# Kernel tuning notes

Hardware: AMD Instinct MI355X
Metric: run time of the kernel (lower is better)

## Reference

```python
import jax, jax.numpy as jnp
import numpy as np
import math

B, S, D = 2, 2048, 2048
H, KVH, HD = 16, 8, 128  # n_heads, n_kv_heads, head_dim
N_REP = H // KVH
ROPE_THETA = 500000.0
NEG_INF = -1e9


def _rope(t, f):
    # t: (B,S,nh,HD) viewed as pairs; f: (S,HD//2,2) = (cos,sin)
    tp = t.reshape(*t.shape[:-1], HD // 2, 2)          # (B,S,nh,HD//2,2)
    fb = f[:, None]                                     # (S,1,HD//2,2)
    row1 = (tp * fb).sum(-1)                            # x0*c + x1*s
    f_rot = jnp.stack([fb[..., 1], -fb[..., 0]], axis=-1)  # (s, -c)
    row0 = (tp * f_rot).sum(-1)                         # x0*s - x1*c
    return jnp.stack([row0, row1], axis=-1).reshape(t.shape)


def setup_inputs() -> dict:
    key = jax.random.key(0)
    ks = jax.random.split(key, 5)
    x = jax.random.normal(ks[0], (B, S, D), dtype=jnp.float32)
    # RoPE table: (S, HD//2, 2) stacked (cos, sin)
    inv_freq = 1.0 / (ROPE_THETA ** (np.arange(0, HD, 2, dtype=np.float32) / HD))
    t = np.arange(S, dtype=np.float32)
    ang = np.outer(t, inv_freq)                         # (S, HD//2)
    freqs_cis = jnp.asarray(np.stack([np.cos(ang), np.sin(ang)], axis=-1))
    # causal additive mask (S,S)
    mask = jnp.where(jnp.triu(jnp.ones((S, S), dtype=bool), k=1), NEG_INF, 0.0).astype(jnp.float32)
    sc = 1.0 / math.sqrt(D)
    wq = jax.random.normal(ks[1], (D, H * HD), dtype=jnp.float32) * sc
    wk = jax.random.normal(ks[2], (D, KVH * HD), dtype=jnp.float32) * sc
    wv = jax.random.normal(ks[3], (D, KVH * HD), dtype=jnp.float32) * sc
    wo = jax.random.normal(ks[4], (H * HD, D), dtype=jnp.float32) * sc
    return {"x": x, "freqs_cis": freqs_cis, "mask": mask, "wq": wq, "wk": wk, "wv": wv, "wo": wo}


def reference(x, freqs_cis, mask, wq, wk, wv, wo):
    bsz, seqlen, _ = x.shape
    xq = (x @ wq).reshape(bsz, seqlen, H, HD)
    xk = (x @ wk).reshape(bsz, seqlen, KVH, HD)
    xv = (x @ wv).reshape(bsz, seqlen, KVH, HD)
    xq = _rope(xq, freqs_cis)
    xk = _rope(xk, freqs_cis)
    keys = jnp.repeat(xk, N_REP, axis=2)                # (B,S,H,HD)
    values = jnp.repeat(xv, N_REP, axis=2)
    q = xq.transpose(0, 2, 1, 3)                        # (B,H,S,HD)
    k = keys.transpose(0, 2, 1, 3)
    v = values.transpose(0, 2, 1, 3)
    scores = jnp.einsum('bhqd,bhkd->bhqk', q, k) / math.sqrt(HD)
    scores = scores + mask                              # broadcast (S,S)
    probs = jax.nn.softmax(scores.astype(jnp.float32), axis=-1).astype(q.dtype)
    out = jnp.einsum('bhqk,bhkd->bhqd', probs, v)
    out = out.transpose(0, 2, 1, 3).reshape(bsz, seqlen, H * HD)
    return out @ wo
```

## Files before the change

### kernel.cpp

```cpp
#include <hip/hip_runtime.h>

typedef short short8 __attribute__((ext_vector_type(8)));
typedef float v4f __attribute__((ext_vector_type(4)));
typedef float v16f __attribute__((ext_vector_type(16)));

#define LOG2E 1.4426950408889634f

__device__ __forceinline__ unsigned short f2bf(float f) {
  unsigned int u = __float_as_uint(f);
  u += 0x7fff + ((u >> 16) & 1);
  return (unsigned short)(u >> 16);
}
__device__ __forceinline__ float b2f(unsigned short h) {
  return __uint_as_float(((unsigned int)h) << 16);
}
__device__ __forceinline__ void gl_lds16(const void* g, void* l) {
  __builtin_amdgcn_global_load_lds((const __attribute__((address_space(1))) void*)g,
                                   (__attribute__((address_space(3))) void*)l, 16, 0, 0);
}

__global__ __launch_bounds__(256) void cvt_f32_bf16(const float* __restrict__ src,
                                                    unsigned short* __restrict__ dst, int n) {
  int i = (blockIdx.x * 256 + threadIdx.x) * 4;
  if (i < n) {
    float4 v = *(const float4*)(src + i);
    ushort4 o;
    o.x = f2bf(v.x); o.y = f2bf(v.y); o.z = f2bf(v.z); o.w = f2bf(v.w);
    *(ushort4*)(dst + i) = o;
  }
}

__global__ __launch_bounds__(256) void transpose_f32_bf16(const float* __restrict__ src,
                                                          unsigned short* __restrict__ dst,
                                                          int srcCols) {
  __shared__ float tile[64][65];
  const int c0 = blockIdx.x * 64;
  const int r0 = blockIdx.y * 64;
  const int t = threadIdx.x;
#pragma unroll
  for (int i = 0; i < 16; ++i) {
    int idx = t + i * 256; int r = idx >> 6, c = idx & 63;
    tile[r][c] = src[(size_t)(r0 + r) * srcCols + c0 + c];
  }
  __syncthreads();
#pragma unroll
  for (int i = 0; i < 16; ++i) {
    int idx = t + i * 256; int r = idx >> 6, c = idx & 63;
    dst[(size_t)(c0 + r) * 2048 + r0 + c] = f2bf(tile[c][r]);
  }
}

template <bool OUT_BF16>
__global__ __launch_bounds__(256) void gemm_bt(const unsigned short* __restrict__ A,
                                               const unsigned short* __restrict__ Bt,
                                               void* __restrict__ Cv,
                                               int M, int N, int K) {
  __shared__ __align__(16) unsigned short As[2][128 * 32];
  __shared__ __align__(16) unsigned short Bs[2][128 * 32];
  const int t = threadIdx.x;
  const int wave = t >> 6, lane = t & 63, quad = lane >> 4, l16 = lane & 15;
  const int tm = blockIdx.y * 128, tn = blockIdx.x * 128;
  const int wm = (wave >> 1) * 64, wn = (wave & 1) * 64;
  v4f acc[4][4];
#pragma unroll
  for (int i = 0; i < 4; ++i)
#pragma unroll
    for (int j = 0; j < 4; ++j) acc[i][j] = (v4f){0.f, 0.f, 0.f, 0.f};

  const int swz = (l16 >> 1) & 3;

  const int s0 = t, s1 = 256 + t;
  const unsigned short* pa0 = A + (size_t)(tm + (s0 >> 2)) * K + ((s0 & 3) ^ ((s0 >> 3) & 3)) * 8;
  const unsigned short* pa1 = A + (size_t)(tm + (s1 >> 2)) * K + ((s1 & 3) ^ ((s1 >> 3) & 3)) * 8;
  const unsigned short* pb0 = Bt + (size_t)(tn + (s0 >> 2)) * K + ((s0 & 3) ^ ((s0 >> 3) & 3)) * 8;
  const unsigned short* pb1 = Bt + (size_t)(tn + (s1 >> 2)) * K + ((s1 & 3) ^ ((s1 >> 3) & 3)) * 8;
  const int dOff0 = (wave * 64) * 8;
  const int dOff1 = (256 + wave * 64) * 8;

  gl_lds16(pa0, &As[0][dOff0]); gl_lds16(pa1, &As[0][dOff1]);
  gl_lds16(pb0, &Bs[0][dOff0]); gl_lds16(pb1, &Bs[0][dOff1]);
  pa0 += 32; pa1 += 32; pb0 += 32; pb1 += 32;

  const int nit = K >> 5;
  for (int it = 0; it < nit; ++it) {
    __syncthreads();
    const int cur = it & 1;
    if (it + 1 < nit) {
      const int nxt = cur ^ 1;
      gl_lds16(pa0, &As[nxt][dOff0]); gl_lds16(pa1, &As[nxt][dOff1]);
      gl_lds16(pb0, &Bs[nxt][dOff0]); gl_lds16(pb1, &Bs[nxt][dOff1]);
      pa0 += 32; pa1 += 32; pb0 += 32; pb1 += 32;
    }
    short8 af[4], bf[4];
#pragma unroll
    for (int mt = 0; mt < 4; ++mt)
      af[mt] = *(const short8*)(&As[cur][(wm + mt * 16 + l16) * 32 + (quad ^ swz) * 8]);
#pragma unroll
    for (int nt = 0; nt < 4; ++nt)
      bf[nt] = *(const short8*)(&Bs[cur][(wn + nt * 16 + l16) * 32 + (quad ^ swz) * 8]);
#pragma unroll
    for (int mt = 0; mt < 4; ++mt)
#pragma unroll
      for (int nt = 0; nt < 4; ++nt)
        acc[mt][nt] = __builtin_amdgcn_mfma_f32_16x16x32_bf16(af[mt], bf[nt], acc[mt][nt], 0, 0, 0);
  }

#pragma unroll
  for (int mt = 0; mt < 4; ++mt)
#pragma unroll
    for (int nt = 0; nt < 4; ++nt)
#pragma unroll
      for (int r = 0; r < 4; ++r) {
        int row = tm + wm + mt * 16 + quad * 4 + r;
        int col = tn + wn + nt * 16 + l16;
        float v = acc[mt][nt][r];
        if (OUT_BF16) ((unsigned short*)Cv)[(size_t)row * N + col] = f2bf(v);
        else          ((float*)Cv)[(size_t)row * N + col] = v;
      }
}

template <bool OUT_BF16>
__global__ __launch_bounds__(512, 2) void gemm256(const unsigned short* __restrict__ A,
                                                  const unsigned short* __restrict__ Bt,
                                                  void* __restrict__ Cv,
                                                  int M, int N, int K) {
  __shared__ __align__(16) unsigned short As[2][256 * 64];
  __shared__ __align__(16) unsigned short Bs[2][256 * 64];
  const int t = threadIdx.x;
  const int wave = t >> 6, lane = t & 63, quad = lane >> 4, l16 = lane & 15;
  const int wr = wave >> 2, wc = wave & 3;

  const int gx = N >> 8;
  int id = blockIdx.y * gridDim.x + blockIdx.x;
  const int nwg = gridDim.x * gridDim.y;
  id = (id & 7) * (nwg >> 3) + (id >> 3);
  const int tm = (id / gx) << 8, tn = (id % gx) << 8;

  v4f acc[8][4];
#pragma unroll
  for (int i = 0; i < 8; ++i)
#pragma unroll
    for (int j = 0; j < 4; ++j) acc[i][j] = (v4f){0.f, 0.f, 0.f, 0.f};

  const int s0 = t, s1 = 512 + t;
  const size_t hA = (size_t)128 * K;
  const unsigned short* a0 = A + (size_t)(tm + (s0 >> 3)) * K + ((s0 & 7) ^ ((s0 >> 3) & 7)) * 8;
  const unsigned short* a1 = A + (size_t)(tm + (s1 >> 3)) * K + ((s1 & 7) ^ ((s1 >> 3) & 7)) * 8;
  const unsigned short* b0 = Bt + (size_t)(tn + (s0 >> 3)) * K + ((s0 & 7) ^ ((s0 >> 3) & 7)) * 8;
  const unsigned short* b1 = Bt + (size_t)(tn + (s1 >> 3)) * K + ((s1 & 7) ^ ((s1 >> 3) & 7)) * 8;
  const int d0 = (wave * 64) * 8;
  const int d1 = (512 + wave * 64) * 8;

#define STG_A(buf, h, koff)                                         \
  do {                                                              \
    gl_lds16(a0 + (size_t)(h) * hA + (koff), &As[buf][(h) * 8192 + d0]); \
    gl_lds16(a1 + (size_t)(h) * hA + (koff), &As[buf][(h) * 8192 + d1]); \
  } while (0)
#define STG_B(buf, h, koff)                                         \
  do {                                                              \
    gl_lds16(b0 + (size_t)(h) * hA + (koff), &Bs[buf][(h) * 8192 + d0]); \
    gl_lds16(b1 + (size_t)(h) * hA + (koff), &Bs[buf][(h) * 8192 + d1]); \
  } while (0)

  const int aBase = (wr * 128 + l16) * 64;
  const int bBase = (wc * 64 + l16) * 64;
  const int c0 = (quad ^ (l16 & 7)) * 8;
  const int c1 = ((4 + quad) ^ (l16 & 7)) * 8;

  const int nkt = K >> 6;

  STG_A(0, 0, 0); STG_A(0, 1, 0);
  STG_B(0, 0, 0); STG_B(0, 1, 0);
  STG_B(1, 0, 64); STG_A(1, 0, 64);
  asm volatile("s_waitcnt vmcnt(4)" ::: "memory");
  __builtin_amdgcn_s_barrier();

  short8 af[4][2], bf[4][2];
  for (int kt = 0; kt < nkt; ++kt) {
    const int cur = kt & 1, nxt = cur ^ 1;
    const int koff = kt << 6;

#pragma unroll
    for (int m = 0; m < 4; ++m) {
      af[m][0] = *(const short8*)(&As[cur][aBase + m * 1024 + c0]);
      af[m][1] = *(const short8*)(&As[cur][aBase + m * 1024 + c1]);
    }
#pragma unroll
    for (int n = 0; n < 2; ++n) {
      bf[n][0] = *(const short8*)(&Bs[cur][bBase + n * 1024 + c0]);
      bf[n][1] = *(const short8*)(&Bs[cur][bBase + n * 1024 + c1]);
    }
    if (kt + 1 < nkt) { STG_A(nxt, 1, koff + 64); STG_B(nxt, 1, koff + 64); }
    __builtin_amdgcn_s_barrier();
    asm volatile("s_waitcnt lgkmcnt(0)" ::: "memory");
    __builtin_amdgcn_s_setprio(1);
#pragma unroll
    for (int m = 0; m < 4; ++m)
#pragma unroll
      for (int n = 0; n < 2; ++n) {
        acc[m][n] = __builtin_amdgcn_mfma_f32_16x16x32_bf16(af[m][0], bf[n][0], acc[m][n], 0, 0, 0);
        acc[m][n] = __builtin_amdgcn_mfma_f32_16x16x32_bf16(af[m][1], bf[n][1], acc[m][n], 0, 0, 0);
      }
    __builtin_amdgcn_s_setprio(0);
    __builtin_amdgcn_s_barrier();

#pragma unroll
    for (int n = 2; n < 4; ++n) {
      bf[n][0] = *(const short8*)(&Bs[cur][bBase + n * 1024 + c0]);
      bf[n][1] = *(const short8*)(&Bs[cur][bBase + n * 1024 + c1]);
    }
    __builtin_amdgcn_s_barrier();
    asm volatile("s_waitcnt lgkmcnt(0)" ::: "memory");
    __builtin_amdgcn_s_setprio(1);
#pragma unroll
    for (int m = 0; m < 4; ++m)
#pragma unroll
      for (int n = 2; n < 4; ++n) {
        acc[m][n] = __builtin_amdgcn_mfma_f32_16x16x32_bf16(af[m][0], bf[n][0], acc[m][n], 0, 0, 0);
        acc[m][n] = __builtin_amdgcn_mfma_f32_16x16x32_bf16(af[m][1], bf[n][1], acc[m][n], 0, 0, 0);
      }
    __builtin_amdgcn_s_setprio(0);
    __builtin_amdgcn_s_barrier();

#pragma unroll
    for (int m = 0; m < 4; ++m) {
      af[m][0] = *(const short8*)(&As[cur][aBase + (4 + m) * 1024 + c0]);
      af[m][1] = *(const short8*)(&As[cur][aBase + (4 + m) * 1024 + c1]);
    }
    if (kt + 2 < nkt) STG_B(cur, 0, koff + 128);
    __builtin_amdgcn_s_barrier();
    asm volatile("s_waitcnt lgkmcnt(0)" ::: "memory");
    __builtin_amdgcn_s_setprio(1);
#pragma unroll
    for (int m = 0; m < 4; ++m)
#pragma unroll
      for (int n = 0; n < 2; ++n) {
        acc[4 + m][n] = __builtin_amdgcn_mfma_f32_16x16x32_bf16(af[m][0], bf[n][0], acc[4 + m][n], 0, 0, 0);
        acc[4 + m][n] = __builtin_amdgcn_mfma_f32_16x16x32_bf16(af[m][1], bf[n][1], acc[4 + m][n], 0, 0, 0);
      }
    __builtin_amdgcn_s_setprio(0);
    __builtin_amdgcn_s_barrier();

    if (kt + 2 < nkt) {
      STG_A(cur, 0, koff + 128);
      asm volatile("s_waitcnt vmcnt(4)" ::: "memory");
    } else {
      asm volatile("s_waitcnt vmcnt(0)" ::: "memory");
    }
    __builtin_amdgcn_s_barrier();
    __builtin_amdgcn_s_setprio(1);
#pragma unroll
    for (int m = 0; m < 4; ++m)
#pragma unroll
      for (int n = 2; n < 4; ++n) {
        acc[4 + m][n] = __builtin_amdgcn_mfma_f32_16x16x32_bf16(af[m][0], bf[n][0], acc[4 + m][n], 0, 0, 0);
        acc[4 + m][n] = __builtin_amdgcn_mfma_f32_16x16x32_bf16(af[m][1], bf[n][1], acc[4 + m][n], 0, 0, 0);
      }
    __builtin_amdgcn_s_setprio(0);
    __builtin_amdgcn_s_barrier();
  }
#undef STG_A
#undef STG_B

#pragma unroll
  for (int mf = 0; mf < 8; ++mf)
#pragma unroll
    for (int nf = 0; nf < 4; ++nf)
#pragma unroll
      for (int r = 0; r < 4; ++r) {
        int row = tm + wr * 128 + mf * 16 + quad * 4 + r;
        int col = tn + wc * 64 + nf * 16 + l16;
        float v = acc[mf][nf][r];
        if (OUT_BF16) ((unsigned short*)Cv)[(size_t)row * N + col] = f2bf(v);
        else          ((float*)Cv)[(size_t)row * N + col] = v;
      }
}

__global__ __launch_bounds__(256) void rope_k(unsigned short* __restrict__ qkv,
                                              const float* __restrict__ freqs) {
  const int bs = blockIdx.x;
  const int s = bs & 2047;
  const float qscale = 0.08838834764831845f;
  unsigned int* row = (unsigned int*)(qkv + (size_t)bs * 4096);
  const float2* fr2 = (const float2*)(freqs + s * 128);
#pragma unroll
  for (int k = 0; k < 6; ++k) {
    int d = threadIdx.x + k * 256;
    float sc = (d < 1024) ? qscale : 1.0f;
    float2 cs = fr2[d & 63];
    unsigned int w = row[d];
    float x0 = b2f((unsigned short)(w & 0xffffu));
    float x1 = b2f((unsigned short)(w >> 16));
    float y0 = (x0 * cs.y - x1 * cs.x) * sc;
    float y1 = (x0 * cs.x + x1 * cs.y) * sc;
    row[d] = ((unsigned int)f2bf(y1) << 16) | (unsigned int)f2bf(y0);
  }
}

__global__ __launch_bounds__(256) void transpose_v(const unsigned short* __restrict__ qkv,
                                                   unsigned short* __restrict__ vt) {
  __shared__ unsigned short tile[64][65];
  const int s0 = blockIdx.x * 64, d0 = blockIdx.y * 64;
  const int bk = blockIdx.z; const int b = bk >> 3, kv = bk & 7;
  const int t = threadIdx.x;
#pragma unroll
  for (int i = 0; i < 16; ++i) {
    int idx = t + i * 256; int r = idx >> 6, c = idx & 63;
    tile[r][c] = qkv[(size_t)(b * 2048 + s0 + r) * 4096 + 3072 + kv * 128 + d0 + c];
  }
  __syncthreads();
#pragma unroll
  for (int i = 0; i < 16; ++i) {
    int idx = t + i * 256; int r = idx >> 6, c = idx & 63;
    vt[((size_t)bk * 128 + d0 + r) * 2048 + s0 + c] = tile[c][r];
  }
}

__global__ __launch_bounds__(256, 2) void attn_k(const unsigned short* __restrict__ qkv,
                                                 const unsigned short* __restrict__ vt,
                                                 unsigned short* __restrict__ Ob) {
  __shared__ __align__(16) unsigned short Ks[2][64 * 128];
  __shared__ __align__(16) unsigned short Vs[2][128 * 64];
  const int t = threadIdx.x, wave = t >> 6, lane = t & 63;
  const int l31 = lane & 31, hh2 = lane >> 5;
  const int hd = blockIdx.y, b = blockIdx.z;
  const int qblk = b ? blockIdx.x : 15 - blockIdx.x;
  const int kv = hd >> 1;
  const int q0 = qblk * 128;
  const int qrel = wave * 32 + l31;
  const int qrow = q0 + qrel;

  auto stage = [&](int jt, int buf) {
#pragma unroll
    for (int issue = 0; issue < 4; ++issue) {
      int s = issue * 256 + t;
      int row = s >> 4;
      int src = ((s & 15) ^ (row & 15)) * 8;
      gl_lds16(qkv + (size_t)(b * 2048 + jt * 64 + row) * 4096 + 2048 + kv * 128 + src,
               &Ks[buf][(issue * 256 + wave * 64) * 8]);
    }
#pragma unroll
    for (int issue = 0; issue < 4; ++issue) {
      int s = issue * 256 + t;
      int row = s >> 3;
      int src = ((s & 7) ^ (row & 7)) * 8;
      gl_lds16(vt + ((size_t)(b * 8 + kv) * 128 + row) * 2048 + jt * 64 + src,
               &Vs[buf][(issue * 256 + wave * 64) * 8]);
    }
  };

  short8 qf[8];
  {
    const unsigned short* qp = qkv + (size_t)(b * 2048 + qrow) * 4096 + hd * 128 + hh2 * 8;
#pragma unroll
    for (int ks = 0; ks < 8; ++ks) qf[ks] = *(const short8*)(qp + ks * 16);
  }
  stage(0, 0);

  v16f oa[4];
#pragma unroll
  for (int i = 0; i < 4; ++i)
#pragma unroll
    for (int r = 0; r < 16; ++r) oa[i][r] = 0.f;
  float m_s = -3.0e38f, l_s = 0.f;

  const int ntl = 2 * (qblk + 1);
  for (int jt = 0; jt < ntl; ++jt) {
    const int cur = jt & 1;
    if (jt + 1 < ntl) {
      stage(jt + 1, cur ^ 1);
      asm volatile("s_waitcnt vmcnt(8)" ::: "memory");
    } else {
      asm volatile("s_waitcnt vmcnt(0)" ::: "memory");
    }
    __builtin_amdgcn_s_barrier();

    v16f st[2];
#pragma unroll
    for (int i = 0; i < 2; ++i)
#pragma unroll
      for (int r = 0; r < 16; ++r) st[i][r] = 0.f;
#pragma unroll
    for (int ks = 0; ks < 8; ++ks)
#pragma unroll
      for (int kt = 0; kt < 2; ++kt) {
        int row = kt * 32 + l31;
        short8 kf = *(const short8*)(
            &Ks[cur][row * 128 + (((ks * 2 + hh2) ^ (row & 15)) * 8)]);
        st[kt] = __builtin_amdgcn_mfma_f32_32x32x16_bf16(kf, qf[ks], st[kt], 0, 0, 0);
      }

    float mx0 = -3.0e38f, mx1 = -3.0e38f;
    if (jt >= 2 * qblk) {
      const int rel = qrel - (jt * 64 - q0);
#pragma unroll
      for (int kt = 0; kt < 2; ++kt)
#pragma unroll
        for (int r = 0; r < 16; ++r) {
          int key = kt * 32 + (r & 3) + 8 * (r >> 2) + 4 * hh2;
          float v = st[kt][r];
          if (key > rel) v = -1.0e30f;
          st[kt][r] = v;
          if (r & 1) mx1 = fmaxf(mx1, v); else mx0 = fmaxf(mx0, v);
        }
    } else {
#pragma unroll
      for (int kt = 0; kt < 2; ++kt)
#pragma unroll
        for (int r = 0; r < 16; ++r) {
          if (r & 1) mx1 = fmaxf(mx1, st[kt][r]); else mx0 = fmaxf(mx0, st[kt][r]);
        }
    }
    float mx = fmaxf(mx0, mx1);
    mx = fmaxf(mx, __shfl_xor(mx, 32));

    if (__ballot(mx > m_s + 8.0f)) {
      float mn = fmaxf(m_s, mx);
      float alpha = exp2f((m_s - mn) * LOG2E);
      m_s = mn;
#pragma unroll
      for (int i = 0; i < 4; ++i)
#pragma unroll
        for (int r = 0; r < 16; ++r) oa[i][r] *= alpha;
      l_s *= alpha;
    }

    float lt0 = 0.f, lt1 = 0.f;
    unsigned int PD[2][8];
#pragma unroll
    for (int kt = 0; kt < 2; ++kt)
#pragma unroll
      for (int j = 0; j < 8; ++j) {
        float p0 = exp2f((st[kt][2 * j]     - m_s) * LOG2E);
        float p1 = exp2f((st[kt][2 * j + 1] - m_s) * LOG2E);
        lt0 += p0; lt1 += p1;
        unsigned int pd;
        asm("v_cvt_pk_bf16_f32 %0, %1, %2" : "=v"(pd) : "v"(p0), "v"(p1));
        PD[kt][j] = pd;
      }
    float lt = lt0 + lt1;
    lt += __shfl_xor(lt, 32);
    l_s += lt;

    unsigned int XD[2][8];
#pragma unroll
    for (int kt = 0; kt < 2; ++kt)
#pragma unroll
      for (int j = 0; j < 8; ++j) XD[kt][j] = __shfl_xor(PD[kt][j], 32);

#pragma unroll
    for (int ks = 0; ks < 4; ++ks) {
      const int tt = ks >> 1, w4 = (ks & 1) * 4;
      union { unsigned int u[4]; short8 s8; } pf;
      pf.u[0] = hh2 ? XD[tt][w4 + 2] : PD[tt][w4 + 0];
      pf.u[1] = hh2 ? XD[tt][w4 + 3] : PD[tt][w4 + 1];
      pf.u[2] = hh2 ? PD[tt][w4 + 2] : XD[tt][w4 + 0];
      pf.u[3] = hh2 ? PD[tt][w4 + 3] : XD[tt][w4 + 1];
#pragma unroll
      for (int dt = 0; dt < 4; ++dt) {
        int row = dt * 32 + l31;
        short8 vf = *(const short8*)(
            &Vs[cur][row * 64 + (((ks * 2 + hh2) ^ (row & 7)) * 8)]);
        oa[dt] = __builtin_amdgcn_mfma_f32_32x32x16_bf16(vf, pf.s8, oa[dt], 0, 0, 0);
      }
    }
    __builtin_amdgcn_s_barrier();
  }

  float inv = 1.0f / l_s;
  unsigned short* orow = Ob + (size_t)(b * 2048 + qrow) * 2048 + hd * 128;
#pragma unroll
  for (int dt = 0; dt < 4; ++dt)
#pragma unroll
    for (int g = 0; g < 4; ++g) {
      ushort4 wv;
      wv.x = f2bf(oa[dt][4 * g + 0] * inv);
      wv.y = f2bf(oa[dt][4 * g + 1] * inv);
      wv.z = f2bf(oa[dt][4 * g + 2] * inv);
      wv.w = f2bf(oa[dt][4 * g + 3] * inv);
      *(ushort4*)(orow + dt * 32 + 8 * g + 4 * hh2) = wv;
    }
}

extern "C" void kernel_launch(void* const* d_in, const int* in_sizes, int n_in,
                              void* d_out, int out_size, void* d_ws, size_t ws_size,
                              hipStream_t stream) {
  (void)in_sizes; (void)n_in; (void)out_size; (void)ws_size;
  const float* x  = (const float*)d_in[0];
  const float* fr = (const float*)d_in[1];
  const float* wq = (const float*)d_in[3];
  const float* wk = (const float*)d_in[4];
  const float* wv = (const float*)d_in[5];
  const float* wo = (const float*)d_in[6];
  float* out = (float*)d_out;

  char* ws = (char*)d_ws;
  unsigned short* Xb    = (unsigned short*)(ws);
  unsigned short* WqkvT = (unsigned short*)(ws + (size_t)(16u << 20));
  unsigned short* WoT   = (unsigned short*)(ws + (size_t)(32u << 20));
  unsigned short* QKV   = (unsigned short*)(ws + (size_t)(40u << 20));
  unsigned short* Vt    = (unsigned short*)(ws);
  unsigned short* Ob    = (unsigned short*)(ws + (size_t)(16u << 20));

  cvt_f32_bf16<<<8192, 256, 0, stream>>>(x, Xb, 2 * 2048 * 2048);
  transpose_f32_bf16<<<dim3(32, 32), 256, 0, stream>>>(wq, WqkvT, 2048);
  transpose_f32_bf16<<<dim3(16, 32), 256, 0, stream>>>(wk, WqkvT + (size_t)2048 * 2048, 1024);
  transpose_f32_bf16<<<dim3(16, 32), 256, 0, stream>>>(wv, WqkvT + (size_t)3072 * 2048, 1024);
  transpose_f32_bf16<<<dim3(32, 32), 256, 0, stream>>>(wo, WoT, 2048);
  gemm256<true><<<dim3(16, 16), 512, 0, stream>>>(Xb, WqkvT, QKV, 4096, 4096, 2048);
  rope_k<<<4096, 256, 0, stream>>>(QKV, fr);
  transpose_v<<<dim3(32, 2, 16), 256, 0, stream>>>(QKV, Vt);
  attn_k<<<dim3(16, 16, 2), 256, 0, stream>>>(QKV, Vt, Ob);
  gemm_bt<false><<<dim3(16, 32), 256, 0, stream>>>(Ob, WoT, out, 4096, 2048, 2048);
}
```

Before: 345.5 us.

## Split causal attention KV range in two and merge partials in combine kernel

Replaces the single attention kernel with a split-KV version: each query block's causal key range is divided into two halves, processed as separate work items. Items are paired per block (item and 1023-item) so each block gets a balanced total workload. The halves write fp32 partial outputs plus max and sum to workspace, and a combine kernel rescales and merges them into bf16. This adds about 64 MB of fp32 partial traffic and an extra launch in exchange for better load balance and more parallel work. It falls back to the old kernel if the workspace is too small.

Measured after the change: 367.6 us. +6.4%, slower.

```diff
diff --git a/kernel.cpp b/kernel.cpp
--- a/kernel.cpp
+++ b/kernel.cpp
@@ -313,6 +313,218 @@
   for (int i = 0; i < 16; ++i) {
     int idx = t + i * 256; int r = idx >> 6, c = idx & 63;
     vt[((size_t)bk * 128 + d0 + r) * 2048 + s0 + c] = tile[c][r];
+  }
+}
+
+__global__ __launch_bounds__(256, 2) void attn_split(const unsigned short* __restrict__ qkv,
+                                                     const unsigned short* __restrict__ vt,
+                                                     float* __restrict__ PO,
+                                                     float* __restrict__ PML) {
+  __shared__ __align__(16) unsigned short Ks[2][64 * 128];
+  __shared__ __align__(16) unsigned short Vs[2][128 * 64];
+  const int t = threadIdx.x, wave = t >> 6, lane = t & 63;
+  const int l31 = lane & 31, hh2 = lane >> 5;
+
+  for (int seg = 0; seg < 2; ++seg) {
+    const int item = seg ? (1023 - (int)blockIdx.x) : (int)blockIdx.x;
+    const int k = 15 - (item >> 6);
+    const int r = item & 63;
+    const int half = r & 1, hb = r >> 1;
+    const int hd = hb & 15, b = hb >> 4;
+    const int kv = hd >> 1;
+    const int q0 = k * 128;
+    const int qrel = wave * 32 + l31;
+    const int qrow = q0 + qrel;
+    const int nt = k + 1, jt0 = half * nt;
+
+    auto stage = [&](int jt, int buf) {
+#pragma unroll
+      for (int issue = 0; issue < 4; ++issue) {
+        int s = issue * 256 + t;
+        int row = s >> 4;
+        int src = ((s & 15) ^ (row & 15)) * 8;
+        gl_lds16(qkv + (size_t)(b * 2048 + jt * 64 + row) * 4096 + 2048 + kv * 128 + src,
+                 &Ks[buf][(issue * 256 + wave * 64) * 8]);
+      }
+#pragma unroll
+      for (int issue = 0; issue < 4; ++issue) {
+        int s = issue * 256 + t;
+        int row = s >> 3;
+        int src = ((s & 7) ^ (row & 7)) * 8;
+        gl_lds16(vt + ((size_t)(b * 8 + kv) * 128 + row) * 2048 + jt * 64 + src,
+                 &Vs[buf][(issue * 256 + wave * 64) * 8]);
+      }
+    };
+
+    short8 qf[8];
+    {
+      const unsigned short* qp = qkv + (size_t)(b * 2048 + qrow) * 4096 + hd * 128 + hh2 * 8;
+#pragma unroll
+      for (int ks = 0; ks < 8; ++ks) qf[ks] = *(const short8*)(qp + ks * 16);
+    }
+    stage(jt0, 0);
+
+    v16f oa[4];
+#pragma unroll
+    for (int i = 0; i < 4; ++i)
+#pragma unroll
+      for (int rr = 0; rr < 16; ++rr) oa[i][rr] = 0.f;
+    float m_s = -3.0e38f, l_s = 0.f;
+
+    for (int u = 0; u < nt; ++u) {
+      const int jt = jt0 + u;
+      const int cur = u & 1;
+      if (u + 1 < nt) {
+        stage(jt + 1, cur ^ 1);
+        asm volatile("s_waitcnt vmcnt(8)" ::: "memory");
+      } else {
+        asm volatile("s_waitcnt vmcnt(0)" ::: "memory");
+      }
+      __builtin_amdgcn_s_barrier();
+
+      v16f st[2];
+#pragma unroll
+      for (int i = 0; i < 2; ++i)
+#pragma unroll
+        for (int rr = 0; rr < 16; ++rr) st[i][rr] = 0.f;
+#pragma unroll
+      for (int ks = 0; ks < 8; ++ks)
+#pragma unroll
+        for (int kt = 0; kt < 2; ++kt) {
+          int row = kt * 32 + l31;
+          short8 kf = *(const short8*)(
+              &Ks[cur][row * 128 + (((ks * 2 + hh2) ^ (row & 15)) * 8)]);
+          st[kt] = __builtin_amdgcn_mfma_f32_32x32x16_bf16(kf, qf[ks], st[kt], 0, 0, 0);
+        }
+
+      float mx0 = -3.0e38f, mx1 = -3.0e38f;
+      if (jt >= 2 * k) {
+        const int rel = qrel - (jt * 64 - q0);
+#pragma unroll
+        for (int kt = 0; kt < 2; ++kt)
+#pragma unroll
+          for (int rr = 0; rr < 16; ++rr) {
+            int key = kt * 32 + (rr & 3) + 8 * (rr >> 2) + 4 * hh2;
+            float v = st[kt][rr];
+            if (key > rel) v = -1.0e30f;
+            st[kt][rr] = v;
+            if (rr & 1) mx1 = fmaxf(mx1, v); else mx0 = fmaxf(mx0, v);
+          }
+      } else {
+#pragma unroll
+        for (int kt = 0; kt < 2; ++kt)
+#pragma unroll
+          for (int rr = 0; rr < 16; ++rr) {
+            if (rr & 1) mx1 = fmaxf(mx1, st[kt][rr]); else mx0 = fmaxf(mx0, st[kt][rr]);
+          }
+      }
+      float mx = fmaxf(mx0, mx1);
+      mx = fmaxf(mx, __shfl_xor(mx, 32));
+
+      if (__ballot(mx > m_s + 8.0f)) {
+        float mn = fmaxf(m_s, mx);
+        float alpha = exp2f((m_s - mn) * LOG2E);
+        m_s = mn;
+#pragma unroll
+        for (int i = 0; i < 4; ++i)
+#pragma unroll
+          for (int rr = 0; rr < 16; ++rr) oa[i][rr] *= alpha;
+        l_s *= alpha;
+      }
+
+      float lt0 = 0.f, lt1 = 0.f;
+      unsigned int PD[2][8];
+#pragma unroll
+      for (int kt = 0; kt < 2; ++kt)
+#pragma unroll
+        for (int j = 0; j < 8; ++j) {
+          float p0 = exp2f((st[kt][2 * j]     - m_s) * LOG2E);
+          float p1 = exp2f((st[kt][2 * j + 1] - m_s) * LOG2E);
+          lt0 += p0; lt1 += p1;
+          unsigned int pd;
+          asm("v_cvt_pk_bf16_f32 %0, %1, %2" : "=v"(pd) : "v"(p0), "v"(p1));
+          PD[kt][j] = pd;
+        }
+      float lt = lt0 + lt1;
+      lt += __shfl_xor(lt, 32);
+      l_s += lt;
+
+      unsigned int XD[2][8];
+#pragma unroll
+      for (int kt = 0; kt < 2; ++kt)
+#pragma unroll
+        for (int j = 0; j < 8; ++j) XD[kt][j] = __shfl_xor(PD[kt][j], 32);
+
+#pragma unroll
+      for (int ks = 0; ks < 4; ++ks) {
+        const int tt = ks >> 1, w4 = (ks & 1) * 4;
+        union { unsigned int u[4]; short8 s8; } pf;
+        pf.u[0] = hh2 ? XD[tt][w4 + 2] : PD[tt][w4 + 0];
+        pf.u[1] = hh2 ? XD[tt][w4 + 3] : PD[tt][w4 + 1];
+        pf.u[2] = hh2 ? PD[tt][w4 + 2] : XD[tt][w4 + 0];
+        pf.u[3] = hh2 ? PD[tt][w4 + 3] : XD[tt][w4 + 1];
+#pragma unroll
+        for (int dt = 0; dt < 4; ++dt) {
+          int row = dt * 32 + l31;
+          short8 vf = *(const short8*)(
+              &Vs[cur][row * 64 + (((ks * 2 + hh2) ^ (row & 7)) * 8)]);
+          oa[dt] = __builtin_amdgcn_mfma_f32_32x32x16_bf16(vf, pf.s8, oa[dt], 0, 0, 0);
+        }
+      }
+      __builtin_amdgcn_s_barrier();
+    }
+
+    float* po = PO + (size_t)item * 16384;
+#pragma unroll
+    for (int dt = 0; dt < 4; ++dt)
+#pragma unroll
+      for (int g = 0; g < 4; ++g) {
+        float4 wv;
+        wv.x = oa[dt][4 * g + 0];
+        wv.y = oa[dt][4 * g + 1];
+        wv.z = oa[dt][4 * g + 2];
+        wv.w = oa[dt][4 * g + 3];
+        *(float4*)(po + qrel * 128 + dt * 32 + 8 * g + 4 * hh2) = wv;
+      }
+    if (hh2 == 0) {
+      PML[item * 256 + qrel] = m_s;
+      PML[item * 256 + 128 + qrel] = l_s;
+    }
+    __syncthreads();
+  }
+}
+
+__global__ __launch_bounds__(256) void combine_k(const float* __restrict__ PO,
+                                                 const float* __restrict__ PML,
+                                                 unsigned short* __restrict__ Ob) {
+  const int cid = blockIdx.x;
+  const int k = 15 - (cid >> 5);
+  const int hb = cid & 31;
+  const int hd = hb & 15, b = hb >> 4;
+  const int i0 = (15 - k) * 64 + hb * 2, i1 = i0 + 1;
+  const int t = threadIdx.x;
+  const int q = t >> 1, dh = (t & 1) * 64;
+
+  float m0 = PML[i0 * 256 + q], l0 = PML[i0 * 256 + 128 + q];
+  float m1 = PML[i1 * 256 + q], l1 = PML[i1 * 256 + 128 + q];
+  float M = fmaxf(m0, m1);
+  float a0 = exp2f((m0 - M) * LOG2E);
+  float a1 = exp2f((m1 - M) * LOG2E);
+  float inv = 1.0f / (a0 * l0 + a1 * l1);
+  a0 *= inv; a1 *= inv;
+
+  const float4* p0 = (const float4*)(PO + (size_t)i0 * 16384 + q * 128 + dh);
+  const float4* p1 = (const float4*)(PO + (size_t)i1 * 16384 + q * 128 + dh);
+  unsigned short* orow = Ob + (size_t)(b * 2048 + k * 128 + q) * 2048 + hd * 128 + dh;
+#pragma unroll
+  for (int j = 0; j < 16; ++j) {
+    float4 x = p0[j], y = p1[j];
+    ushort4 w;
+    w.x = f2bf(a0 * x.x + a1 * y.x);
+    w.y = f2bf(a0 * x.y + a1 * y.y);
+    w.z = f2bf(a0 * x.z + a1 * y.z);
+    w.w = f2bf(a0 * x.w + a1 * y.w);
+    *(ushort4*)(orow + j * 4) = w;
   }
 }
 
@@ -485,7 +697,7 @@
 extern "C" void kernel_launch(void* const* d_in, const int* in_sizes, int n_in,
                               void* d_out, int out_size, void* d_ws, size_t ws_size,
                               hipStream_t stream) {
-  (void)in_sizes; (void)n_in; (void)out_size; (void)ws_size;
+  (void)in_sizes; (void)n_in; (void)out_size;
   const float* x  = (const float*)d_in[0];
   const float* fr = (const float*)d_in[1];
   const float* wq = (const float*)d_in[3];
@@ -501,6 +713,9 @@
   unsigned short* QKV   = (unsigned short*)(ws + (size_t)(40u << 20));
   unsigned short* Vt    = (unsigned short*)(ws);
   unsigned short* Ob    = (unsigned short*)(ws + (size_t)(16u << 20));
+  const size_t PO_off  = (size_t)72 << 20;
+  const size_t PML_off = PO_off + ((size_t)64 << 20);
+  const size_t ws_need = PML_off + ((size_t)2 << 20);
 
   cvt_f32_bf16<<<8192, 256, 0, stream>>>(x, Xb, 2 * 2048 * 2048);
   transpose_f32_bf16<<<dim3(32, 32), 256, 0, stream>>>(wq, WqkvT, 2048);
@@ -510,6 +725,13 @@
   gemm256<true><<<dim3(16, 16), 512, 0, stream>>>(Xb, WqkvT, QKV, 4096, 4096, 2048);
   rope_k<<<4096, 256, 0, stream>>>(QKV, fr);
   transpose_v<<<dim3(32, 2, 16), 256, 0, stream>>>(QKV, Vt);
-  attn_k<<<dim3(16, 16, 2), 256, 0, stream>>>(QKV, Vt, Ob);
+  if (ws_size >= ws_need) {
+    float* PO  = (float*)(ws + PO_off);
+    float* PML = (float*)(ws + PML_off);
+    attn_split<<<512, 256, 0, stream>>>(QKV, Vt, PO, PML);
+    combine_k<<<512, 256, 0, stream>>>(PO, PML, Ob);
+  } else {
+    attn_k<<<dim3(16, 16, 2), 256, 0, stream>>>(QKV, Vt, Ob);
+  }
   gemm_bt<false><<<dim3(16, 32), 256, 0, stream>>>(Ob, WoT, out, 4096, 2048, 2048);
 }
```
